# Kernel optimization log

Hardware: AMD Instinct MI355X
Metric: run time of the kernel (lower is better)

The kernel has to match this reference:

```python
import jax, jax.numpy as jnp
import numpy as np

H = 128  # hidden_size

def setup_inputs() -> dict:
    key = jax.random.key(0)
    ks = jax.random.split(key, 12)
    B, SEQ = 256, 1000
    static = jax.random.normal(ks[0], (B, 2, SEQ), jnp.float32)
    dynamic = jax.random.uniform(ks[1], (B, 2, SEQ), jnp.float32)
    # Encoder = 1x1 Conv1d(in_ch -> H): weight (H, in_ch), bias (H,)
    def xavier(k, shape):
        fan_in, fan_out = shape[1], shape[0]
        lim = np.sqrt(6.0 / (fan_in + fan_out)).astype(np.float32)
        return jax.random.uniform(k, shape, jnp.float32, -lim, lim)
    enc_s_w = xavier(ks[2], (H, 2)); enc_s_b = jnp.zeros((H,), jnp.float32)
    enc_d_w = xavier(ks[3], (H, 2)); enc_d_b = jnp.zeros((H,), jnp.float32)
    v = xavier(ks[4], (1, H))[0]                 # attention vector (H,)
    W = xavier(ks[5], (H, 3 * H))                # attention matrix (H, 3H)
    dense_w = xavier(ks[6], (H, 128)); dense_b = jnp.zeros((H,), jnp.float32)
    lin_w = xavier(ks[7], (1, H)); lin_b = jnp.zeros((1,), jnp.float32)
    return {"static": static, "dynamic": dynamic,
            "enc_s_w": enc_s_w, "enc_s_b": enc_s_b,
            "enc_d_w": enc_d_w, "enc_d_b": enc_d_b,
            "v": v, "W": W,
            "dense_w": dense_w, "dense_b": dense_b,
            "lin_w": lin_w, "lin_b": lin_b}


def reference(static, dynamic, enc_s_w, enc_s_b, enc_d_w, enc_d_b,
              v, W, dense_w, dense_b, lin_w, lin_b):
    B = static.shape[0]
    # 1x1-conv encoders (computed once; identical across loop iterations)
    e = jnp.einsum('hc,bcs->bhs', enc_s_w, static) + enc_s_b[None, :, None]   # (B,H,S)
    dyn_ld = jnp.broadcast_to(dynamic[:, 1:2, :], dynamic.shape)              # load channel expanded
    d = jnp.einsum('hc,bcs->bhs', enc_d_w, dyn_ld) + enc_d_b[None, :, None]   # (B,H,S)
    hy = jnp.zeros((B, H), static.dtype)
    for _ in range(3):  # fixed 3-step refinement loop
        hidden = jnp.concatenate(
            [e, d, jnp.broadcast_to(hy[:, :, None], e.shape)], axis=1)        # (B,3H,S)
        u = jnp.tanh(jnp.einsum('hk,bks->bhs', W, hidden))                    # (B,H,S)
        logit = jnp.einsum('h,bhs->bs', v, u)                                 # (B,S)
        prob = jax.nn.softmax(logit, axis=-1)
        hy = jnp.einsum('bs,bhs->bh', prob, e)                                # context update
    out = jax.nn.relu(hy @ dense_w.T + dense_b) @ lin_w.T + lin_b             # (B,1)
    return out
```

## Files before the change

### kernel.cpp

```cpp
#include <hip/hip_runtime.h>
#include <math.h>

#define HH 128
#define SS 1000
#define NT 1024
#define NW (NT / 64)

#define C1 2.8853900817779268f
#define C2 1.4426950408889634f

__device__ __forceinline__ void pin(float& x) { asm volatile("" : "+v"(x)); }

template <int CTRL>
__device__ __forceinline__ float dpp_add(float x) {
    int s = __builtin_amdgcn_update_dpp(0, __builtin_bit_cast(int, x),
                                        CTRL, 0xF, 0xF, true);
    return x + __builtin_bit_cast(float, s);
}

__global__ __launch_bounds__(NT, 4) void sc_fused(
    const float* __restrict__ stat, const float* __restrict__ dyn,
    const float* __restrict__ enc_s_w, const float* __restrict__ enc_s_b,
    const float* __restrict__ enc_d_w, const float* __restrict__ enc_d_b,
    const float* __restrict__ v, const float* __restrict__ W,
    const float* __restrict__ dense_w, const float* __restrict__ dense_b,
    const float* __restrict__ lin_w, const float* __restrict__ lin_b,
    float* __restrict__ out) {
    const int b    = blockIdx.x;
    const int t    = threadIdx.x;
    const int wave = t >> 6;
    const int lane = t & 63;
    const int g    = t & 15;
    const int sg   = t >> 4;

    __shared__ float part[7][8][HH];
    __shared__ __align__(16) float4 xs[NT];
    __shared__ __align__(16) float kc[8][HH];
    __shared__ float4 red4[2][NW];
    __shared__ float hy_sh[HH];
    __shared__ float svc2_sh;

    {
        float x0 = 0.f, x1 = 0.f, yv = 0.f;
        if (t < SS) {
            const float* sb = stat + (size_t)b * 2 * SS;
            x0 = sb[t];
            x1 = sb[SS + t];
            yv = dyn[(size_t)b * 2 * SS + SS + t];
        }
        xs[t] = make_float4(x0, x1, yv, 0.f);
    }

    {
        const int h = t & (HH - 1);
        const int q = t >> 7;
        const float4* W1 = (const float4*)(W + h * (3 * HH));
        const float4* W2 = (const float4*)(W + h * (3 * HH) + HH);
        const float4* W3 = (const float4*)(W + h * (3 * HH) + 2 * HH);
        const float4* ES = (const float4*)enc_s_w;
        const float4* ED = (const float4*)enc_d_w;
        const float4* SB = (const float4*)enc_s_b;
        const float4* DB = (const float4*)enc_d_b;
        float a0 = 0.f, a1 = 0.f, ad = 0.f, cc = 0.f, w30 = 0.f, w31 = 0.f, w3b = 0.f;
        #pragma unroll
        for (int k4 = q * 4; k4 < q * 4 + 4; ++k4) {
            float4 w1 = W1[k4], w2 = W2[k4], w3 = W3[k4];
            float4 e01 = ES[2 * k4], e23 = ES[2 * k4 + 1];
            float4 d01 = ED[2 * k4], d23 = ED[2 * k4 + 1];
            float4 sb = SB[k4], db = DB[k4];
            a0 = fmaf(w1.x, e01.x, a0); a0 = fmaf(w1.y, e01.z, a0);
            a0 = fmaf(w1.z, e23.x, a0); a0 = fmaf(w1.w, e23.z, a0);
            a1 = fmaf(w1.x, e01.y, a1); a1 = fmaf(w1.y, e01.w, a1);
            a1 = fmaf(w1.z, e23.y, a1); a1 = fmaf(w1.w, e23.w, a1);
            ad = fmaf(w2.x, d01.x + d01.y, ad); ad = fmaf(w2.y, d01.z + d01.w, ad);
            ad = fmaf(w2.z, d23.x + d23.y, ad); ad = fmaf(w2.w, d23.z + d23.w, ad);
            cc = fmaf(w1.x, sb.x, cc); cc = fmaf(w1.y, sb.y, cc);
            cc = fmaf(w1.z, sb.z, cc); cc = fmaf(w1.w, sb.w, cc);
            cc = fmaf(w2.x, db.x, cc); cc = fmaf(w2.y, db.y, cc);
            cc = fmaf(w2.z, db.z, cc); cc = fmaf(w2.w, db.w, cc);
            w30 = fmaf(w3.x, e01.x, w30); w30 = fmaf(w3.y, e01.z, w30);
            w30 = fmaf(w3.z, e23.x, w30); w30 = fmaf(w3.w, e23.z, w30);
            w31 = fmaf(w3.x, e01.y, w31); w31 = fmaf(w3.y, e01.w, w31);
            w31 = fmaf(w3.z, e23.y, w31); w31 = fmaf(w3.w, e23.w, w31);
            w3b = fmaf(w3.x, sb.x, w3b); w3b = fmaf(w3.y, sb.y, w3b);
            w3b = fmaf(w3.z, sb.z, w3b); w3b = fmaf(w3.w, sb.w, w3b);
        }
        part[0][q][h] = a0;  part[1][q][h] = a1;  part[2][q][h] = ad;
        part[3][q][h] = cc;  part[4][q][h] = w30; part[5][q][h] = w31;
        part[6][q][h] = w3b;
    }
    __syncthreads();

    if (t < HH) {
        float r0 = 0.f, r1 = 0.f, r2 = 0.f, r3 = 0.f, r4 = 0.f, r5 = 0.f, r6 = 0.f;
        #pragma unroll
        for (int q = 0; q < 8; ++q) {
            r0 += part[0][q][t]; r1 += part[1][q][t]; r2 += part[2][q][t];
            r3 += part[3][q][t]; r4 += part[4][q][t]; r5 += part[5][q][t];
            r6 += part[6][q][t];
        }
        kc[0][t] = r0 * C1;
        kc[1][t] = r1 * C1;
        kc[2][t] = r2 * C1;
        kc[3][t] = v[t];
        kc[4][t] = r3 * C1;
        kc[5][t] = (r3 + r6) * C1;
        kc[6][t] = r4 * C1;
        kc[7][t] = r5 * C1;
    } else if (t < 160) {
        int j = t - 128;
        float4 x = ((const float4*)v)[j];
        float s = (x.x + x.y) + (x.z + x.w);
        #pragma unroll
        for (int off = 1; off < 32; off <<= 1) s += __shfl_xor(s, off);
        if (t == 128) svc2_sh = s * C2;
    }
    __syncthreads();

    const int h0 = g * 8;
    float4 f;
    f = *(const float4*)&kc[0][h0];     float a00 = f.x, a01 = f.y, a02 = f.z, a03 = f.w;
    f = *(const float4*)&kc[0][h0 + 4]; float a04 = f.x, a05 = f.y, a06 = f.z, a07 = f.w;
    f = *(const float4*)&kc[1][h0];     float a10 = f.x, a11 = f.y, a12 = f.z, a13 = f.w;
    f = *(const float4*)&kc[1][h0 + 4]; float a14 = f.x, a15 = f.y, a16 = f.z, a17 = f.w;
    f = *(const float4*)&kc[2][h0];     float ad0 = f.x, ad1 = f.y, ad2 = f.z, ad3 = f.w;
    f = *(const float4*)&kc[2][h0 + 4]; float ad4 = f.x, ad5 = f.y, ad6 = f.z, ad7 = f.w;
    f = *(const float4*)&kc[3][h0];     float vv0 = f.x, vv1 = f.y, vv2 = f.z, vv3 = f.w;
    f = *(const float4*)&kc[3][h0 + 4]; float vv4 = f.x, vv5 = f.y, vv6 = f.z, vv7 = f.w;
    pin(a00); pin(a01); pin(a02); pin(a03); pin(a04); pin(a05); pin(a06); pin(a07);
    pin(a10); pin(a11); pin(a12); pin(a13); pin(a14); pin(a15); pin(a16); pin(a17);
    pin(ad0); pin(ad1); pin(ad2); pin(ad3); pin(ad4); pin(ad5); pin(ad6); pin(ad7);
    pin(vv0); pin(vv1); pin(vv2); pin(vv3); pin(vv4); pin(vv5); pin(vv6); pin(vv7);
    float svc2 = svc2_sh;
    pin(svc2);

    float X0 = 0.f, X1 = 0.f;

    auto run_iter = [&](int iter, int parity) {
        float cg0, cg1, cg2, cg3, cg4, cg5, cg6, cg7;
        if (iter == 0) {
            float4 lo = *(const float4*)&kc[4][h0];
            float4 hi = *(const float4*)&kc[4][h0 + 4];
            cg0 = lo.x; cg1 = lo.y; cg2 = lo.z; cg3 = lo.w;
            cg4 = hi.x; cg5 = hi.y; cg6 = hi.z; cg7 = hi.w;
        } else {
            float4 cbl = *(const float4*)&kc[5][h0];
            float4 cbh = *(const float4*)&kc[5][h0 + 4];
            float4 w0l = *(const float4*)&kc[6][h0];
            float4 w0h = *(const float4*)&kc[6][h0 + 4];
            float4 w1l = *(const float4*)&kc[7][h0];
            float4 w1h = *(const float4*)&kc[7][h0 + 4];
            cg0 = fmaf(w0l.x, X0, fmaf(w1l.x, X1, cbl.x));
            cg1 = fmaf(w0l.y, X0, fmaf(w1l.y, X1, cbl.y));
            cg2 = fmaf(w0l.z, X0, fmaf(w1l.z, X1, cbl.z));
            cg3 = fmaf(w0l.w, X0, fmaf(w1l.w, X1, cbl.w));
            cg4 = fmaf(w0h.x, X0, fmaf(w1h.x, X1, cbh.x));
            cg5 = fmaf(w0h.y, X0, fmaf(w1h.y, X1, cbh.y));
            cg6 = fmaf(w0h.z, X0, fmaf(w1h.z, X1, cbh.z));
            cg7 = fmaf(w0h.w, X0, fmaf(w1h.w, X1, cbh.w));
        }
        pin(cg0); pin(cg1); pin(cg2); pin(cg3);
        pin(cg4); pin(cg5); pin(cg6); pin(cg7);

        float S = 0.f, Sx0 = 0.f, Sx1 = 0.f;
        #pragma unroll 4
        for (int pass = 0; pass < 16; ++pass) {
            const int s = pass * 64 + sg;
            float4 x = xs[s];
            float z0 = fmaf(a00, x.x, fmaf(a10, x.y, fmaf(ad0, x.z, cg0)));
            float z1 = fmaf(a01, x.x, fmaf(a11, x.y, fmaf(ad1, x.z, cg1)));
            float z2 = fmaf(a02, x.x, fmaf(a12, x.y, fmaf(ad2, x.z, cg2)));
            float z3 = fmaf(a03, x.x, fmaf(a13, x.y, fmaf(ad3, x.z, cg3)));
            float z4 = fmaf(a04, x.x, fmaf(a14, x.y, fmaf(ad4, x.z, cg4)));
            float z5 = fmaf(a05, x.x, fmaf(a15, x.y, fmaf(ad5, x.z, cg5)));
            float z6 = fmaf(a06, x.x, fmaf(a16, x.y, fmaf(ad6, x.z, cg6)));
            float z7 = fmaf(a07, x.x, fmaf(a17, x.y, fmaf(ad7, x.z, cg7)));
            float e0 = __builtin_amdgcn_exp2f(z0);
            float e1 = __builtin_amdgcn_exp2f(z1);
            float e2 = __builtin_amdgcn_exp2f(z2);
            float e3 = __builtin_amdgcn_exp2f(z3);
            float e4 = __builtin_amdgcn_exp2f(z4);
            float e5 = __builtin_amdgcn_exp2f(z5);
            float e6 = __builtin_amdgcn_exp2f(z6);
            float e7 = __builtin_amdgcn_exp2f(z7);
            float acc;
            acc = fmaf(vv0, __builtin_amdgcn_rcpf(1.f + e0), 0.f);
            acc = fmaf(vv1, __builtin_amdgcn_rcpf(1.f + e1), acc);
            acc = fmaf(vv2, __builtin_amdgcn_rcpf(1.f + e2), acc);
            acc = fmaf(vv3, __builtin_amdgcn_rcpf(1.f + e3), acc);
            acc = fmaf(vv4, __builtin_amdgcn_rcpf(1.f + e4), acc);
            acc = fmaf(vv5, __builtin_amdgcn_rcpf(1.f + e5), acc);
            acc = fmaf(vv6, __builtin_amdgcn_rcpf(1.f + e6), acc);
            acc = fmaf(vv7, __builtin_amdgcn_rcpf(1.f + e7), acc);
            acc = dpp_add<0x118>(acc);
            acc = dpp_add<0x114>(acc);
            acc = dpp_add<0x112>(acc);
            acc = dpp_add<0x111>(acc);
            const bool own = (g == 15) && (s < SS);
            float arg = own ? fmaf(-C1, acc, svc2) : -200.f;
            float p = __builtin_amdgcn_exp2f(arg);
            S   += p;
            Sx0  = fmaf(p, x.x, Sx0);
            Sx1  = fmaf(p, x.y, Sx1);
        }
        S   += __shfl_xor(S, 16);   S   += __shfl_xor(S, 32);
        Sx0 += __shfl_xor(Sx0, 16); Sx0 += __shfl_xor(Sx0, 32);
        Sx1 += __shfl_xor(Sx1, 16); Sx1 += __shfl_xor(Sx1, 32);
        if (lane == 15) red4[parity][wave] = make_float4(S, Sx0, Sx1, 0.f);
        __syncthreads();
        float4 w4 = red4[parity][lane & 15];
        #pragma unroll
        for (int off = 1; off < 16; off <<= 1) {
            w4.x += __shfl_xor(w4.x, off);
            w4.y += __shfl_xor(w4.y, off);
            w4.z += __shfl_xor(w4.z, off);
        }
        float inv = __builtin_amdgcn_rcpf(w4.x);
        X0 = w4.y * inv;
        X1 = w4.z * inv;
    };

    run_iter(0, 0);
    run_iter(1, 1);
    run_iter(2, 0);

    if (t < HH)
        hy_sh[t] = fmaf(enc_s_w[2 * t], X0, fmaf(enc_s_w[2 * t + 1], X1, enc_s_b[t]));
    __syncthreads();

    float o = 0.f;
    if (t < HH) {
        const float4* dw4 = (const float4*)(dense_w + t * HH);
        const float4* hy4 = (const float4*)hy_sh;
        float r = dense_b[t];
        #pragma unroll 4
        for (int k = 0; k < HH / 4; ++k) {
            float4 d4 = dw4[k], h4 = hy4[k];
            r = fmaf(d4.x, h4.x, fmaf(d4.y, h4.y, fmaf(d4.z, h4.z, fmaf(d4.w, h4.w, r))));
        }
        o = lin_w[t] * fmaxf(r, 0.f);
    }
    #pragma unroll
    for (int off = 32; off > 0; off >>= 1) o += __shfl_xor(o, off);
    if (lane == 0) red4[0][wave].x = o;
    __syncthreads();
    if (t == 0) {
        float s = 0.f;
        for (int i = 0; i < NW; ++i) s += red4[0][i].x;
        out[b] = s + lin_b[0];
    }
}

extern "C" void kernel_launch(void* const* d_in, const int* in_sizes, int n_in,
                              void* d_out, int out_size, void* d_ws, size_t ws_size,
                              hipStream_t stream) {
    const float* stat    = (const float*)d_in[0];
    const float* dyn     = (const float*)d_in[1];
    const float* enc_s_w = (const float*)d_in[2];
    const float* enc_s_b = (const float*)d_in[3];
    const float* enc_d_w = (const float*)d_in[4];
    const float* enc_d_b = (const float*)d_in[5];
    const float* v       = (const float*)d_in[6];
    const float* W       = (const float*)d_in[7];
    const float* dense_w = (const float*)d_in[8];
    const float* dense_b = (const float*)d_in[9];
    const float* lin_w   = (const float*)d_in[10];
    const float* lin_b   = (const float*)d_in[11];
    float* out = (float*)d_out;

    const int B = in_sizes[0] / (2 * SS);

    hipLaunchKernelGGL(sc_fused, dim3(B), dim3(NT), 0, stream,
                       stat, dyn, enc_s_w, enc_s_b, enc_d_w, enc_d_b, v, W,
                       dense_w, dense_b, lin_w, lin_b, out);
}
```

Measured before the change: 47.96 us.

## Use packed float2 FMAs with 16 hidden units per lane over 8 lanes

Each lane now handles 16 hidden units instead of 8, processed as pairs with float2 vector FMAs that can map to packed-FP32 instructions. The inner loop shrinks from 16 to 8 passes and is fully unrolled, and the cross-lane DPP reduction drops one step because only 8 lanes share a sequence position. The aim is fewer FMA issue slots and less reduction overhead per position. The exp and rcp calls stay scalar, and the doubled weight set increases register pressure under the 1024-thread launch bound.

```diff
diff --git a/kernel.cpp b/kernel.cpp
--- a/kernel.cpp
+++ b/kernel.cpp
@@ -9,7 +9,10 @@
 #define C1 2.8853900817779268f
 #define C2 1.4426950408889634f
 
-__device__ __forceinline__ void pin(float& x) { asm volatile("" : "+v"(x)); }
+typedef float v2f __attribute__((ext_vector_type(2)));
+
+__device__ __forceinline__ void pinf(float& x) { asm volatile("" : "+v"(x)); }
+__device__ __forceinline__ void pin2(v2f& x)   { asm volatile("" : "+v"(x)); }
 
 template <int CTRL>
 __device__ __forceinline__ float dpp_add(float x) {
@@ -17,6 +20,36 @@
                                         CTRL, 0xF, 0xF, true);
     return x + __builtin_bit_cast(float, s);
 }
+
+#define LD16(P, ROW)                                                         \
+    {                                                                        \
+        const float4* p4_ = (const float4*)&kc[ROW][h0];                     \
+        float4 u0_ = p4_[0], u1_ = p4_[1], u2_ = p4_[2], u3_ = p4_[3];       \
+        P##0 = (v2f){u0_.x, u0_.y}; P##1 = (v2f){u0_.z, u0_.w};              \
+        P##2 = (v2f){u1_.x, u1_.y}; P##3 = (v2f){u1_.z, u1_.w};              \
+        P##4 = (v2f){u2_.x, u2_.y}; P##5 = (v2f){u2_.z, u2_.w};              \
+        P##6 = (v2f){u3_.x, u3_.y}; P##7 = (v2f){u3_.z, u3_.w};              \
+    }
+
+#define PIN8(P) { pin2(P##0); pin2(P##1); pin2(P##2); pin2(P##3);            \
+                  pin2(P##4); pin2(P##5); pin2(P##6); pin2(P##7); }
+
+#define HPAIR(J)                                                             \
+    {                                                                        \
+        v2f z_ = __builtin_elementwise_fma(                                  \
+            a0_##J, vx0,                                                     \
+            __builtin_elementwise_fma(                                       \
+                a1_##J, vx1,                                                 \
+                __builtin_elementwise_fma(ad_##J, vyv, cg_##J)));            \
+        v2f e_;                                                              \
+        e_.x = __builtin_amdgcn_exp2f(z_.x);                                 \
+        e_.y = __builtin_amdgcn_exp2f(z_.y);                                 \
+        v2f d_ = e_ + one2;                                                  \
+        v2f r_;                                                              \
+        r_.x = __builtin_amdgcn_rcpf(d_.x);                                  \
+        r_.y = __builtin_amdgcn_rcpf(d_.y);                                  \
+        acc2 = __builtin_elementwise_fma(vv_##J, r_, acc2);                  \
+    }
 
 __global__ __launch_bounds__(NT, 4) void sc_fused(
     const float* __restrict__ stat, const float* __restrict__ dyn,
@@ -30,8 +63,8 @@
     const int t    = threadIdx.x;
     const int wave = t >> 6;
     const int lane = t & 63;
-    const int g    = t & 15;
-    const int sg   = t >> 4;
+    const int g8   = t & 7;
+    const int sg   = t >> 3;
 
     __shared__ float part[7][8][HH];
     __shared__ __align__(16) float4 xs[NT];
@@ -117,96 +150,65 @@
     }
     __syncthreads();
 
-    const int h0 = g * 8;
-    float4 f;
-    f = *(const float4*)&kc[0][h0];     float a00 = f.x, a01 = f.y, a02 = f.z, a03 = f.w;
-    f = *(const float4*)&kc[0][h0 + 4]; float a04 = f.x, a05 = f.y, a06 = f.z, a07 = f.w;
-    f = *(const float4*)&kc[1][h0];     float a10 = f.x, a11 = f.y, a12 = f.z, a13 = f.w;
-    f = *(const float4*)&kc[1][h0 + 4]; float a14 = f.x, a15 = f.y, a16 = f.z, a17 = f.w;
-    f = *(const float4*)&kc[2][h0];     float ad0 = f.x, ad1 = f.y, ad2 = f.z, ad3 = f.w;
-    f = *(const float4*)&kc[2][h0 + 4]; float ad4 = f.x, ad5 = f.y, ad6 = f.z, ad7 = f.w;
-    f = *(const float4*)&kc[3][h0];     float vv0 = f.x, vv1 = f.y, vv2 = f.z, vv3 = f.w;
-    f = *(const float4*)&kc[3][h0 + 4]; float vv4 = f.x, vv5 = f.y, vv6 = f.z, vv7 = f.w;
-    pin(a00); pin(a01); pin(a02); pin(a03); pin(a04); pin(a05); pin(a06); pin(a07);
-    pin(a10); pin(a11); pin(a12); pin(a13); pin(a14); pin(a15); pin(a16); pin(a17);
-    pin(ad0); pin(ad1); pin(ad2); pin(ad3); pin(ad4); pin(ad5); pin(ad6); pin(ad7);
-    pin(vv0); pin(vv1); pin(vv2); pin(vv3); pin(vv4); pin(vv5); pin(vv6); pin(vv7);
+    const int h0 = g8 * 16;
+    v2f a0_0, a0_1, a0_2, a0_3, a0_4, a0_5, a0_6, a0_7;
+    v2f a1_0, a1_1, a1_2, a1_3, a1_4, a1_5, a1_6, a1_7;
+    v2f ad_0, ad_1, ad_2, ad_3, ad_4, ad_5, ad_6, ad_7;
+    v2f vv_0, vv_1, vv_2, vv_3, vv_4, vv_5, vv_6, vv_7;
+    LD16(a0_, 0); LD16(a1_, 1); LD16(ad_, 2); LD16(vv_, 3);
+    PIN8(a0_); PIN8(a1_); PIN8(ad_); PIN8(vv_);
     float svc2 = svc2_sh;
-    pin(svc2);
+    pinf(svc2);
+    const v2f one2 = {1.f, 1.f};
+    const bool owner = (g8 == 7);
 
     float X0 = 0.f, X1 = 0.f;
 
     auto run_iter = [&](int iter, int parity) {
-        float cg0, cg1, cg2, cg3, cg4, cg5, cg6, cg7;
+        v2f cg_0, cg_1, cg_2, cg_3, cg_4, cg_5, cg_6, cg_7;
         if (iter == 0) {
-            float4 lo = *(const float4*)&kc[4][h0];
-            float4 hi = *(const float4*)&kc[4][h0 + 4];
-            cg0 = lo.x; cg1 = lo.y; cg2 = lo.z; cg3 = lo.w;
-            cg4 = hi.x; cg5 = hi.y; cg6 = hi.z; cg7 = hi.w;
+            LD16(cg_, 4);
         } else {
-            float4 cbl = *(const float4*)&kc[5][h0];
-            float4 cbh = *(const float4*)&kc[5][h0 + 4];
-            float4 w0l = *(const float4*)&kc[6][h0];
-            float4 w0h = *(const float4*)&kc[6][h0 + 4];
-            float4 w1l = *(const float4*)&kc[7][h0];
-            float4 w1h = *(const float4*)&kc[7][h0 + 4];
-            cg0 = fmaf(w0l.x, X0, fmaf(w1l.x, X1, cbl.x));
-            cg1 = fmaf(w0l.y, X0, fmaf(w1l.y, X1, cbl.y));
-            cg2 = fmaf(w0l.z, X0, fmaf(w1l.z, X1, cbl.z));
-            cg3 = fmaf(w0l.w, X0, fmaf(w1l.w, X1, cbl.w));
-            cg4 = fmaf(w0h.x, X0, fmaf(w1h.x, X1, cbh.x));
-            cg5 = fmaf(w0h.y, X0, fmaf(w1h.y, X1, cbh.y));
-            cg6 = fmaf(w0h.z, X0, fmaf(w1h.z, X1, cbh.z));
-            cg7 = fmaf(w0h.w, X0, fmaf(w1h.w, X1, cbh.w));
-        }
-        pin(cg0); pin(cg1); pin(cg2); pin(cg3);
-        pin(cg4); pin(cg5); pin(cg6); pin(cg7);
+            v2f cb_0, cb_1, cb_2, cb_3, cb_4, cb_5, cb_6, cb_7;
+            v2f w0_0, w0_1, w0_2, w0_3, w0_4, w0_5, w0_6, w0_7;
+            v2f w1_0, w1_1, w1_2, w1_3, w1_4, w1_5, w1_6, w1_7;
+            LD16(cb_, 5); LD16(w0_, 6); LD16(w1_, 7);
+            v2f X0v = {X0, X0}, X1v = {X1, X1};
+            cg_0 = __builtin_elementwise_fma(w0_0, X0v, __builtin_elementwise_fma(w1_0, X1v, cb_0));
+            cg_1 = __builtin_elementwise_fma(w0_1, X0v, __builtin_elementwise_fma(w1_1, X1v, cb_1));
+            cg_2 = __builtin_elementwise_fma(w0_2, X0v, __builtin_elementwise_fma(w1_2, X1v, cb_2));
+            cg_3 = __builtin_elementwise_fma(w0_3, X0v, __builtin_elementwise_fma(w1_3, X1v, cb_3));
+            cg_4 = __builtin_elementwise_fma(w0_4, X0v, __builtin_elementwise_fma(w1_4, X1v, cb_4));
+            cg_5 = __builtin_elementwise_fma(w0_5, X0v, __builtin_elementwise_fma(w1_5, X1v, cb_5));
+            cg_6 = __builtin_elementwise_fma(w0_6, X0v, __builtin_elementwise_fma(w1_6, X1v, cb_6));
+            cg_7 = __builtin_elementwise_fma(w0_7, X0v, __builtin_elementwise_fma(w1_7, X1v, cb_7));
+        }
+        PIN8(cg_);
 
         float S = 0.f, Sx0 = 0.f, Sx1 = 0.f;
-        #pragma unroll 4
-        for (int pass = 0; pass < 16; ++pass) {
-            const int s = pass * 64 + sg;
+        #pragma unroll
+        for (int pass = 0; pass < 8; ++pass) {
+            const int s = pass * 128 + sg;
             float4 x = xs[s];
-            float z0 = fmaf(a00, x.x, fmaf(a10, x.y, fmaf(ad0, x.z, cg0)));
-            float z1 = fmaf(a01, x.x, fmaf(a11, x.y, fmaf(ad1, x.z, cg1)));
-            float z2 = fmaf(a02, x.x, fmaf(a12, x.y, fmaf(ad2, x.z, cg2)));
-            float z3 = fmaf(a03, x.x, fmaf(a13, x.y, fmaf(ad3, x.z, cg3)));
-            float z4 = fmaf(a04, x.x, fmaf(a14, x.y, fmaf(ad4, x.z, cg4)));
-            float z5 = fmaf(a05, x.x, fmaf(a15, x.y, fmaf(ad5, x.z, cg5)));
-            float z6 = fmaf(a06, x.x, fmaf(a16, x.y, fmaf(ad6, x.z, cg6)));
-            float z7 = fmaf(a07, x.x, fmaf(a17, x.y, fmaf(ad7, x.z, cg7)));
-            float e0 = __builtin_amdgcn_exp2f(z0);
-            float e1 = __builtin_amdgcn_exp2f(z1);
-            float e2 = __builtin_amdgcn_exp2f(z2);
-            float e3 = __builtin_amdgcn_exp2f(z3);
-            float e4 = __builtin_amdgcn_exp2f(z4);
-            float e5 = __builtin_amdgcn_exp2f(z5);
-            float e6 = __builtin_amdgcn_exp2f(z6);
-            float e7 = __builtin_amdgcn_exp2f(z7);
-            float acc;
-            acc = fmaf(vv0, __builtin_amdgcn_rcpf(1.f + e0), 0.f);
-            acc = fmaf(vv1, __builtin_amdgcn_rcpf(1.f + e1), acc);
-            acc = fmaf(vv2, __builtin_amdgcn_rcpf(1.f + e2), acc);
-            acc = fmaf(vv3, __builtin_amdgcn_rcpf(1.f + e3), acc);
-            acc = fmaf(vv4, __builtin_amdgcn_rcpf(1.f + e4), acc);
-            acc = fmaf(vv5, __builtin_amdgcn_rcpf(1.f + e5), acc);
-            acc = fmaf(vv6, __builtin_amdgcn_rcpf(1.f + e6), acc);
-            acc = fmaf(vv7, __builtin_amdgcn_rcpf(1.f + e7), acc);
-            acc = dpp_add<0x118>(acc);
+            v2f vx0 = {x.x, x.x}, vx1 = {x.y, x.y}, vyv = {x.z, x.z};
+            v2f acc2 = {0.f, 0.f};
+            HPAIR(0); HPAIR(1); HPAIR(2); HPAIR(3);
+            HPAIR(4); HPAIR(5); HPAIR(6); HPAIR(7);
+            float acc = acc2.x + acc2.y;
             acc = dpp_add<0x114>(acc);
             acc = dpp_add<0x112>(acc);
             acc = dpp_add<0x111>(acc);
-            const bool own = (g == 15) && (s < SS);
+            const bool own = owner && (s < SS);
             float arg = own ? fmaf(-C1, acc, svc2) : -200.f;
             float p = __builtin_amdgcn_exp2f(arg);
             S   += p;
             Sx0  = fmaf(p, x.x, Sx0);
             Sx1  = fmaf(p, x.y, Sx1);
         }
-        S   += __shfl_xor(S, 16);   S   += __shfl_xor(S, 32);
-        Sx0 += __shfl_xor(Sx0, 16); Sx0 += __shfl_xor(Sx0, 32);
-        Sx1 += __shfl_xor(Sx1, 16); Sx1 += __shfl_xor(Sx1, 32);
-        if (lane == 15) red4[parity][wave] = make_float4(S, Sx0, Sx1, 0.f);
+        S   += __shfl_xor(S, 8);   S   += __shfl_xor(S, 16);   S   += __shfl_xor(S, 32);
+        Sx0 += __shfl_xor(Sx0, 8); Sx0 += __shfl_xor(Sx0, 16); Sx0 += __shfl_xor(Sx0, 32);
+        Sx1 += __shfl_xor(Sx1, 8); Sx1 += __shfl_xor(Sx1, 16); Sx1 += __shfl_xor(Sx1, 32);
+        if (lane == 7) red4[parity][wave] = make_float4(S, Sx0, Sx1, 0.f);
         __syncthreads();
         float4 w4 = red4[parity][lane & 15];
         #pragma unroll
```

Result: faster. 43.01 us (-10.3%).
